# Kernel tuning notes

Hardware: AMD Instinct MI355X
Metric: run time of the kernel (lower is better)

## Reference

```python
import jax, jax.numpy as jnp
import numpy as np

N = 500_000       # nodes
E = 8_000_000     # edges (avg degree 16)
IN_DIM = 16       # node_in_dim
HID = 32          # DCRNN hidden (hard-coded in RecurrentGCN)
OUT_DIM = 8       # node_out_dim


def setup_inputs() -> dict:
    key = jax.random.key(0)
    ks = jax.random.split(key, 12)
    scale_g = 1.0 / np.sqrt(IN_DIM + HID)  # glorot-ish for DConv weights
    scale_l = 1.0 / np.sqrt(HID)
    return {
        "x": jax.random.normal(ks[0], (N, IN_DIM), jnp.float32),
        "edge_index": jax.random.randint(ks[1], (2, E), 0, N, jnp.int32),
        "edge_weight": jax.random.uniform(ks[2], (E,), jnp.float32),
        "h": jnp.zeros((N, HID), jnp.float32),
        # DConv weights: original shape (2, K=1, in, out); K=1 -> store (2, in, out)
        "w_z": jax.random.normal(ks[3], (2, IN_DIM + HID, HID), jnp.float32) * scale_g,
        "b_z": jnp.zeros((HID,), jnp.float32),
        "w_r": jax.random.normal(ks[4], (2, IN_DIM + HID, HID), jnp.float32) * scale_g,
        "b_r": jnp.zeros((HID,), jnp.float32),
        "w_h": jax.random.normal(ks[5], (2, IN_DIM + HID, HID), jnp.float32) * scale_g,
        "b_h": jnp.zeros((HID,), jnp.float32),
        "w_lin": jax.random.normal(ks[6], (HID, OUT_DIM), jnp.float32) * scale_l,
        "b_lin": jnp.zeros((OUT_DIM,), jnp.float32),
    }


def _dconv_k1(xh, w, b):
    # DConv with K=1: only the Chebyshev k=0 term survives:
    #   H = X @ W[0,0] + X @ W[1,0] + b  (out-diffusion + in-diffusion weights)
    # edge_index / edge_weight do not enter the math for K=1.
    return xh @ (w[0] + w[1]) + b


def reference(x, edge_index, edge_weight, h, w_z, b_z, w_r, b_r, w_h, b_h, w_lin, b_lin):
    # DCRNN GRU cell (h=None in torch -> zeros, supplied explicitly here)
    xh = jnp.concatenate([x, h], axis=1)                  # [N, IN+HID]
    z = jax.nn.sigmoid(_dconv_k1(xh, w_z, b_z))           # update gate [N, HID]
    r = jax.nn.sigmoid(_dconv_k1(xh, w_r, b_r))           # reset gate  [N, HID]
    xhr = jnp.concatenate([x, h * r], axis=1)             # [N, IN+HID]
    h_tilde = jnp.tanh(_dconv_k1(xhr, w_h, b_h))          # candidate   [N, HID]
    h_new = z * h + (1.0 - z) * h_tilde                   # [N, HID]
    out = jax.nn.relu(h_new) @ w_lin + b_lin              # [N, OUT_DIM]
    return (out, h_new)
```

## Files before the change

### kernel.cpp

```cpp
#include <hip/hip_runtime.h>


#define N_NODES 500000
#define IN_DIM  16
#define HID     32
#define OUT_DIM 8
#define XH      48
#define NTILES  31250
#define HFS     36

typedef unsigned int u32;
typedef unsigned short u16;
typedef __attribute__((ext_vector_type(8))) short bf16x8;
typedef __attribute__((ext_vector_type(4))) float f32x4;

static __device__ __forceinline__ float bfbits(u32 hi){ union{u32 x; float f;} t; t.x=hi; return t.f; }
static __device__ __forceinline__ float bflo(u32 u){ return bfbits(u<<16); }
static __device__ __forceinline__ float bfhi(u32 u){ return bfbits(u & 0xffff0000u); }
static __device__ __forceinline__ float bf2f(u16 s){ return bfbits(((u32)s)<<16); }
static __device__ __forceinline__ u16 f2bf(float f){
    union{float f;u32 x;} t; t.f=f; u32 x=t.x;
    return (u16)((x + 0x7fffu + ((x>>16)&1u)) >> 16);
}
static __device__ __forceinline__ u32 cvtpk(float a, float b){
    u32 r; asm("v_cvt_pk_bf16_f32 %0, %1, %2" : "=v"(r) : "v"(a), "v"(b)); return r;
}
static __device__ __forceinline__ float sigm(float a){
    return 1.f / (1.f + __expf(-a));
}
static __device__ __forceinline__ float tanh_(float a){
    float e = __expf(-2.f * fabsf(a));
    float t = (1.f - e) / (1.f + e);
    return __builtin_copysignf(t, a);
}

#define LFENCE() asm volatile("s_waitcnt lgkmcnt(0)" ::: "memory")
#define MFMA16(a,b,c) __builtin_amdgcn_mfma_f32_16x16x32_bf16(a,b,c,0,0,0)

static __device__ __forceinline__ float ldf(const void* p, int i, bool F32){
    return F32 ? ((const float*)p)[i] : bf2f(((const u16*)p)[i]);
}
static __device__ __forceinline__ float wsum(const void* wp, int k, int c, bool F32){
    int i0 = k*HID + c;
    return ldf(wp, i0, F32) + ldf(wp, XH*HID + i0, F32);
}
static __device__ __forceinline__ char* stgp(char* base, int row, int off){
    return base + row*128 + (off ^ ((row & 7) << 4));
}

__global__ __launch_bounds__(256)
void rgcn_kernel(const void* __restrict__ xp_,
                 const void* __restrict__ hp_,
                 const void* __restrict__ wz_, const void* __restrict__ bz_,
                 const void* __restrict__ wr_, const void* __restrict__ br_,
                 const void* __restrict__ wh_, const void* __restrict__ bh_,
                 const void* __restrict__ wl_, const void* __restrict__ bl_,
                 void* __restrict__ dout_)
{
    __shared__ u16   sStage[4][16*64];
    __shared__ float sHf[4][16*HFS];
    __shared__ int sF32;

    const int tid = threadIdx.x;

    if (tid == 0) {
        const u32* xw = (const u32*)xp_;
        int f = 0;
        for (int q = 0; q < 128; q++) {
            float lo = bflo(xw[q]);
            if (!(fabsf(lo) <= 1e6f)) { f = 1; break; }
        }
        sF32 = f;
    }
    __syncthreads();
    const bool F32 = (sF32 != 0);

    const int lane = tid & 63, wv = tid >> 6;
    const int c16 = lane & 15, g = lane >> 4;
    const int row4 = lane >> 2, q4 = lane & 3;
    char*  stage = (char*)sStage[wv];
    float* hf    = sHf[wv];

    char* pXw = stgp(stage, row4, q4*8);
    char* pHw = stgp(stage, row4, 32 + q4*16);
    float* pHfw = hf + row4*HFS + q4*8;
    char* pA0 = stgp(stage, c16, 16*g);
    char* pA1 = stgp(stage, c16, 64 + 16*g);
    char* pPairH[4]; char* pPairR[4]; const float* pHfr[4];
#pragma unroll
    for (int rr = 0; rr < 4; rr++) {
        int nl = g*4 + rr;
        pPairH[rr] = stgp(stage, nl, 32 + 4*c16);
        pPairR[rr] = stgp(stage, nl, 4*c16);
        pHfr[rr]   = hf + nl*HFS + 2*c16;
    }

    {
        uint2 z2; z2.x = 0u; z2.y = 0u;
        *(uint2*)stgp(stage, row4, 96 + q4*8) = z2;
    }

    float bzv[2], brv[2], bhv[2];
#pragma unroll
    for (int tt = 0; tt < 2; tt++) {
        bzv[tt] = ldf(bz_, 2*c16 + tt, F32);
        brv[tt] = ldf(br_, 2*c16 + tt, F32);
        bhv[tt] = ldf(bh_, 2*c16 + tt, F32);
    }
    float blv = (c16 < OUT_DIM) ? ldf(bl_, c16, F32) : 0.f;

    bf16x8 Bz[2][2], Br[2][2], Bh[2][2], Bl;
#pragma unroll
    for (int kt = 0; kt < 2; kt++) {
#pragma unroll
        for (int tt = 0; tt < 2; tt++) {
            union { u16 us[8]; bf16x8 v; } uz, ur, uh;
#pragma unroll
            for (int e = 0; e < 8; e++) {
                int k = kt*32 + g*8 + e;
                int c = 2*c16 + tt;
                float vz = 0.f, vr = 0.f, vh = 0.f;
                if (k < XH) {
                    vz = wsum(wz_, k, c, F32);
                    vr = wsum(wr_, k, c, F32);
                    vh = wsum(wh_, k, c, F32);
                }
                uz.us[e] = f2bf(vz); ur.us[e] = f2bf(vr); uh.us[e] = f2bf(vh);
            }
            Bz[kt][tt] = uz.v; Br[kt][tt] = ur.v; Bh[kt][tt] = uh.v;
        }
    }
    {
        union { u16 us[8]; bf16x8 v; } ul;
#pragma unroll
        for (int e = 0; e < 8; e++) {
            int k = g*8 + e;
            float v = (c16 < OUT_DIM) ? ldf(wl_, k*OUT_DIM + c16, F32) : 0.f;
            ul.us[e] = f2bf(v);
        }
        Bl = ul.v;
    }

    float* outF = (float*)dout_;
    float* hnF  = outF + (size_t)N_NODES * OUT_DIM;
    u16*   outB = (u16*)dout_;
    u16*   hnB  = outB + (size_t)N_NODES * OUT_DIM;

    const int wid = blockIdx.x*4 + wv;
    const int nw  = gridDim.x*4;

    for (int t = wid; t < NTILES; t += nw) {
        const size_t nb = (size_t)t * 16;

        if (F32) {
            const float* xb = (const float*)xp_ + nb*IN_DIM;
            float4 xv = *(const float4*)(xb + row4*IN_DIM + q4*4);
            uint2 xp2; xp2.x = cvtpk(xv.x, xv.y); xp2.y = cvtpk(xv.z, xv.w);
            *(uint2*)pXw = xp2;
            const float* hb = (const float*)hp_ + nb*HID;
            float4 h0 = *(const float4*)(hb + row4*HID + q4*8);
            float4 h1 = *(const float4*)(hb + row4*HID + q4*8 + 4);
            uint4 hp4; hp4.x = cvtpk(h0.x,h0.y); hp4.y = cvtpk(h0.z,h0.w);
            hp4.z = cvtpk(h1.x,h1.y); hp4.w = cvtpk(h1.z,h1.w);
            *(uint4*)pHw = hp4;
            *(float4*)pHfw = h0; *(float4*)(pHfw + 4) = h1;
        } else {
            const u16* xb = (const u16*)xp_ + nb*IN_DIM;
            *(uint2*)pXw = *(const uint2*)(xb + row4*IN_DIM + q4*4);
            const u16* hb = (const u16*)hp_ + nb*HID;
            *(uint4*)pHw = *(const uint4*)(hb + row4*HID + q4*8);
        }
        LFENCE();

        bf16x8 a0 = *(const bf16x8*)pA0;
        bf16x8 a1 = *(const bf16x8*)pA1;

        f32x4 accZ[2], accR[2];
#pragma unroll
        for (int tt = 0; tt < 2; tt++) {
            f32x4 az; az[0]=bzv[tt]; az[1]=bzv[tt]; az[2]=bzv[tt]; az[3]=bzv[tt];
            az = MFMA16(a0, Bz[0][tt], az);
            az = MFMA16(a1, Bz[1][tt], az);
            accZ[tt] = az;
            f32x4 ar; ar[0]=brv[tt]; ar[1]=brv[tt]; ar[2]=brv[tt]; ar[3]=brv[tt];
            ar = MFMA16(a0, Br[0][tt], ar);
            ar = MFMA16(a1, Br[1][tt], ar);
            accR[tt] = ar;
        }

        float z0a[4], z1a[4], hv0[4], hv1[4];
#pragma unroll
        for (int rr = 0; rr < 4; rr++) {
            float h0, h1;
            if (F32) {
                float2 hp2 = *(const float2*)pHfr[rr];
                h0 = hp2.x; h1 = hp2.y;
            } else {
                u32 hw = *(const u32*)pPairH[rr];
                h0 = bflo(hw); h1 = bfhi(hw);
            }
            hv0[rr] = h0; hv1[rr] = h1;
            float z0 = sigm(accZ[0][rr]), z1 = sigm(accZ[1][rr]);
            z0a[rr] = z0; z1a[rr] = z1;
            float r0 = sigm(accR[0][rr]), r1 = sigm(accR[1][rr]);
            *(u32*)pPairH[rr] = cvtpk(h0*r0, h1*r1);
        }
        LFENCE();

        bf16x8 b0 = *(const bf16x8*)pA0;
        bf16x8 b1 = *(const bf16x8*)pA1;
        f32x4 accH[2];
#pragma unroll
        for (int tt = 0; tt < 2; tt++) {
            f32x4 ah; ah[0]=bhv[tt]; ah[1]=bhv[tt]; ah[2]=bhv[tt]; ah[3]=bhv[tt];
            ah = MFMA16(b0, Bh[0][tt], ah);
            ah = MFMA16(b1, Bh[1][tt], ah);
            accH[tt] = ah;
        }

#pragma unroll
        for (int rr = 0; rr < 4; rr++) {
            int nl = g*4 + rr;
            float t0 = tanh_(accH[0][rr]), t1 = tanh_(accH[1][rr]);
            float n0 = t0 + z0a[rr]*(hv0[rr] - t0);
            float n1 = t1 + z1a[rr]*(hv1[rr] - t1);
            *(u32*)pPairR[rr] = cvtpk(fmaxf(n0, 0.f), fmaxf(n1, 0.f));
            if (F32) {
                float2 st; st.x = n0; st.y = n1;
                *(float2*)(hnF + (nb + nl)*HID + 2*c16) = st;
            } else {
                *(u32*)(hnB + (nb + nl)*HID + 2*c16) = cvtpk(n0, n1);
            }
        }
        LFENCE();

        bf16x8 a3 = *(const bf16x8*)pA0;
        f32x4 accO; accO[0]=blv; accO[1]=blv; accO[2]=blv; accO[3]=blv;
        accO = MFMA16(a3, Bl, accO);
        if (c16 < OUT_DIM) {
            if (F32) {
#pragma unroll
                for (int rr = 0; rr < 4; rr++)
                    outF[(nb + g*4 + rr)*OUT_DIM + c16] = accO[rr];
            } else {
#pragma unroll
                for (int rr = 0; rr < 4; rr++)
                    outB[(nb + g*4 + rr)*OUT_DIM + c16] = (u16)(cvtpk(accO[rr], accO[rr]) & 0xffffu);
            }
        }
    }
}

extern "C" void kernel_launch(void* const* d_in, const int* in_sizes, int n_in,
                              void* d_out, int out_size, void* d_ws, size_t ws_size,
                              hipStream_t stream) {
    const int block = 256;
    const int grid  = 2048;
    rgcn_kernel<<<grid, block, 0, stream>>>(
        d_in[0], d_in[3], d_in[4], d_in[5], d_in[6], d_in[7],
        d_in[8], d_in[9], d_in[10], d_in[11], d_out);
}
```

Baseline: 262.0 us.

## Prefetch next tile into registers, stage summed weights in LDS, drop fp32 h copy

Loads for the next tile's x and h are now issued into registers before the current tile is computed, so global-memory latency overlaps with the MFMA and activation work. The per-lane build of the B weight fragments, which did many scattered global loads, is replaced by a cooperative build of bf16 summed weights in LDS followed by vector LDS reads. The format check is spread over a wavefront with a ballot. The separate fp32 copy of h in LDS is removed, and h is now read back from the bf16 stage, which lowers the precision of h used in the gate update.

```diff
diff --git a/kernel.cpp b/kernel.cpp
--- a/kernel.cpp
+++ b/kernel.cpp
@@ -7,7 +7,7 @@
 #define OUT_DIM 8
 #define XH      48
 #define NTILES  31250
-#define HFS     36
+#define WROW    72
 
 typedef unsigned int u32;
 typedef unsigned short u16;
@@ -18,12 +18,14 @@
 static __device__ __forceinline__ float bflo(u32 u){ return bfbits(u<<16); }
 static __device__ __forceinline__ float bfhi(u32 u){ return bfbits(u & 0xffff0000u); }
 static __device__ __forceinline__ float bf2f(u16 s){ return bfbits(((u32)s)<<16); }
+static __device__ __forceinline__ float u2f(u32 u){ union{u32 x; float f;} t; t.x=u; return t.f; }
+static __device__ __forceinline__ u32 f2u(float f){ union{float f;u32 x;} t; t.f=f; return t.x; }
+static __device__ __forceinline__ u32 cvtpk(float a, float b){
+    u32 r; asm("v_cvt_pk_bf16_f32 %0, %1, %2" : "=v"(r) : "v"(a), "v"(b)); return r;
+}
 static __device__ __forceinline__ u16 f2bf(float f){
     union{float f;u32 x;} t; t.f=f; u32 x=t.x;
     return (u16)((x + 0x7fffu + ((x>>16)&1u)) >> 16);
-}
-static __device__ __forceinline__ u32 cvtpk(float a, float b){
-    u32 r; asm("v_cvt_pk_bf16_f32 %0, %1, %2" : "=v"(r) : "v"(a), "v"(b)); return r;
 }
 static __device__ __forceinline__ float sigm(float a){
     return 1.f / (1.f + __expf(-a));
@@ -57,42 +59,57 @@
                  const void* __restrict__ wl_, const void* __restrict__ bl_,
                  void* __restrict__ dout_)
 {
-    __shared__ u16   sStage[4][16*64];
-    __shared__ float sHf[4][16*HFS];
+    __shared__ u16 sW[3][32*WROW];
+    __shared__ u16 sStage[4][16*64];
     __shared__ int sF32;
 
     const int tid = threadIdx.x;
 
-    if (tid == 0) {
+    if (tid < 64) {
         const u32* xw = (const u32*)xp_;
-        int f = 0;
-        for (int q = 0; q < 128; q++) {
-            float lo = bflo(xw[q]);
-            if (!(fabsf(lo) <= 1e6f)) { f = 1; break; }
-        }
-        sF32 = f;
+        int bad = 0;
+#pragma unroll
+        for (int q = 0; q < 2; q++) {
+            float lo = bflo(xw[tid*2 + q]);
+            if (!(fabsf(lo) <= 1e6f)) bad = 1;
+        }
+        unsigned long long m = __ballot(bad);
+        if (tid == 0) sF32 = (m != 0ull) ? 1 : 0;
     }
     __syncthreads();
     const bool F32 = (sF32 != 0);
+
+    {
+        const void* wsrc[3] = { wz_, wr_, wh_ };
+#pragma unroll
+        for (int m = 0; m < 3; m++) {
+            u32* dst = (u32*)sW[m];
+            for (int o = tid; o < 32*(WROW/2); o += 256) {
+                int c = o / (WROW/2), kk = o - c*(WROW/2);
+                int k0 = 2*kk, k1 = 2*kk + 1;
+                float v0 = (k0 < XH) ? wsum(wsrc[m], k0, c, F32) : 0.f;
+                float v1 = (k1 < XH) ? wsum(wsrc[m], k1, c, F32) : 0.f;
+                dst[o] = cvtpk(v0, v1);
+            }
+        }
+    }
+    __syncthreads();
 
     const int lane = tid & 63, wv = tid >> 6;
     const int c16 = lane & 15, g = lane >> 4;
     const int row4 = lane >> 2, q4 = lane & 3;
-    char*  stage = (char*)sStage[wv];
-    float* hf    = sHf[wv];
+    char* stage = (char*)sStage[wv];
 
     char* pXw = stgp(stage, row4, q4*8);
     char* pHw = stgp(stage, row4, 32 + q4*16);
-    float* pHfw = hf + row4*HFS + q4*8;
     char* pA0 = stgp(stage, c16, 16*g);
     char* pA1 = stgp(stage, c16, 64 + 16*g);
-    char* pPairH[4]; char* pPairR[4]; const float* pHfr[4];
+    char* pPairH[4]; char* pPairR[4];
 #pragma unroll
     for (int rr = 0; rr < 4; rr++) {
         int nl = g*4 + rr;
         pPairH[rr] = stgp(stage, nl, 32 + 4*c16);
         pPairR[rr] = stgp(stage, nl, 4*c16);
-        pHfr[rr]   = hf + nl*HFS + 2*c16;
     }
 
     {
@@ -114,20 +131,10 @@
     for (int kt = 0; kt < 2; kt++) {
 #pragma unroll
         for (int tt = 0; tt < 2; tt++) {
-            union { u16 us[8]; bf16x8 v; } uz, ur, uh;
-#pragma unroll
-            for (int e = 0; e < 8; e++) {
-                int k = kt*32 + g*8 + e;
-                int c = 2*c16 + tt;
-                float vz = 0.f, vr = 0.f, vh = 0.f;
-                if (k < XH) {
-                    vz = wsum(wz_, k, c, F32);
-                    vr = wsum(wr_, k, c, F32);
-                    vh = wsum(wh_, k, c, F32);
-                }
-                uz.us[e] = f2bf(vz); ur.us[e] = f2bf(vr); uh.us[e] = f2bf(vh);
-            }
-            Bz[kt][tt] = uz.v; Br[kt][tt] = ur.v; Bh[kt][tt] = uh.v;
+            int boff = (2*c16 + tt)*(WROW*2) + (kt*32 + g*8)*2;
+            Bz[kt][tt] = *(const bf16x8*)((const char*)sW[0] + boff);
+            Br[kt][tt] = *(const bf16x8*)((const char*)sW[1] + boff);
+            Bh[kt][tt] = *(const bf16x8*)((const char*)sW[2] + boff);
         }
     }
     {
@@ -149,31 +156,55 @@
     const int wid = blockIdx.x*4 + wv;
     const int nw  = gridDim.x*4;
 
+    float4 pfx, pfh0, pfh1;
+#define PLOAD(TT) do { \
+        size_t nbp = (size_t)(TT) * 16; \
+        if (F32) { \
+            const float* xb = (const float*)xp_ + nbp*IN_DIM; \
+            pfx  = *(const float4*)(xb + row4*IN_DIM + q4*4); \
+            const float* hb = (const float*)hp_ + nbp*HID; \
+            pfh0 = *(const float4*)(hb + row4*HID + q4*8); \
+            pfh1 = *(const float4*)(hb + row4*HID + q4*8 + 4); \
+        } else { \
+            const u16* xb = (const u16*)xp_ + nbp*IN_DIM; \
+            uint2 xv = *(const uint2*)(xb + row4*IN_DIM + q4*4); \
+            pfx.x = u2f(xv.x); pfx.y = u2f(xv.y); \
+            const u16* hb = (const u16*)hp_ + nbp*HID; \
+            uint4 hv = *(const uint4*)(hb + row4*HID + q4*8); \
+            pfh0.x = u2f(hv.x); pfh0.y = u2f(hv.y); pfh0.z = u2f(hv.z); pfh0.w = u2f(hv.w); \
+        } \
+    } while (0)
+
+    if (wid < NTILES) PLOAD(wid);
+
     for (int t = wid; t < NTILES; t += nw) {
         const size_t nb = (size_t)t * 16;
 
         if (F32) {
-            const float* xb = (const float*)xp_ + nb*IN_DIM;
-            float4 xv = *(const float4*)(xb + row4*IN_DIM + q4*4);
-            uint2 xp2; xp2.x = cvtpk(xv.x, xv.y); xp2.y = cvtpk(xv.z, xv.w);
+            uint2 xp2; xp2.x = cvtpk(pfx.x, pfx.y); xp2.y = cvtpk(pfx.z, pfx.w);
             *(uint2*)pXw = xp2;
-            const float* hb = (const float*)hp_ + nb*HID;
-            float4 h0 = *(const float4*)(hb + row4*HID + q4*8);
-            float4 h1 = *(const float4*)(hb + row4*HID + q4*8 + 4);
-            uint4 hp4; hp4.x = cvtpk(h0.x,h0.y); hp4.y = cvtpk(h0.z,h0.w);
-            hp4.z = cvtpk(h1.x,h1.y); hp4.w = cvtpk(h1.z,h1.w);
+            uint4 hp4; hp4.x = cvtpk(pfh0.x, pfh0.y); hp4.y = cvtpk(pfh0.z, pfh0.w);
+            hp4.z = cvtpk(pfh1.x, pfh1.y); hp4.w = cvtpk(pfh1.z, pfh1.w);
             *(uint4*)pHw = hp4;
-            *(float4*)pHfw = h0; *(float4*)(pHfw + 4) = h1;
         } else {
-            const u16* xb = (const u16*)xp_ + nb*IN_DIM;
-            *(uint2*)pXw = *(const uint2*)(xb + row4*IN_DIM + q4*4);
-            const u16* hb = (const u16*)hp_ + nb*HID;
-            *(uint4*)pHw = *(const uint4*)(hb + row4*HID + q4*8);
+            uint2 xp2; xp2.x = f2u(pfx.x); xp2.y = f2u(pfx.y);
+            *(uint2*)pXw = xp2;
+            uint4 hp4; hp4.x = f2u(pfh0.x); hp4.y = f2u(pfh0.y);
+            hp4.z = f2u(pfh0.z); hp4.w = f2u(pfh0.w);
+            *(uint4*)pHw = hp4;
+        }
+
+        {
+            int tn = t + nw;
+            if (tn < NTILES) PLOAD(tn);
         }
         LFENCE();
 
         bf16x8 a0 = *(const bf16x8*)pA0;
         bf16x8 a1 = *(const bf16x8*)pA1;
+        u32 hwp[4];
+#pragma unroll
+        for (int rr = 0; rr < 4; rr++) hwp[rr] = *(const u32*)pPairH[rr];
 
         f32x4 accZ[2], accR[2];
 #pragma unroll
@@ -191,14 +222,7 @@
         float z0a[4], z1a[4], hv0[4], hv1[4];
 #pragma unroll
         for (int rr = 0; rr < 4; rr++) {
-            float h0, h1;
-            if (F32) {
-                float2 hp2 = *(const float2*)pHfr[rr];
-                h0 = hp2.x; h1 = hp2.y;
-            } else {
-                u32 hw = *(const u32*)pPairH[rr];
-                h0 = bflo(hw); h1 = bfhi(hw);
-            }
+            float h0 = bflo(hwp[rr]), h1 = bfhi(hwp[rr]);
             hv0[rr] = h0; hv1[rr] = h1;
             float z0 = sigm(accZ[0][rr]), z1 = sigm(accZ[1][rr]);
             z0a[rr] = z0; z1a[rr] = z1;
@@ -249,6 +273,7 @@
             }
         }
     }
+#undef PLOAD
 }
 
 extern "C" void kernel_launch(void* const* d_in, const int* in_sizes, int n_in,
```

Result: faster. 252.5 us (-3.6%).
